# Kernel optimization log

Hardware: AMD Instinct MI355X
Metric: run time of the kernel (lower is better)

The kernel has to match this reference:

```python
import jax, jax.numpy as jnp
import numpy as np

NUM_JOINTS = 24
NUM_THETAS = NUM_JOINTS * 3  # 72
NUM_VERTS = 6890
NUM_BETAS = 10
BATCH = 512

SMPL_PARENTS = np.array([0, 0, 0, 0, 1, 2, 3, 4, 5, 6, 7, 8, 9, 9, 9,
                         12, 13, 14, 16, 17, 18, 19, 20, 21], dtype=np.int32)


def setup_inputs() -> dict:
    key = jax.random.key(0)
    ks = jax.random.split(key, 6)
    x = jax.random.normal(ks[0], (BATCH, NUM_THETAS + NUM_BETAS), dtype=jnp.float32) * 0.3
    v_template = jax.random.normal(ks[1], (NUM_VERTS, 3), dtype=jnp.float32) * 0.3
    shapedirs = jax.random.normal(ks[2], (NUM_BETAS, NUM_VERTS * 3), dtype=jnp.float32) * 0.01
    posedirs = jax.random.normal(ks[3], (207, NUM_VERTS * 3), dtype=jnp.float32) * 0.001
    Jr = jax.random.uniform(ks[4], (NUM_VERTS, NUM_JOINTS), dtype=jnp.float32)
    J_regressor = Jr / jnp.sum(Jr, axis=0, keepdims=True)
    W = jax.random.uniform(ks[5], (NUM_VERTS, NUM_JOINTS), dtype=jnp.float32)
    lbs_weights = W / jnp.sum(W, axis=1, keepdims=True)  # rows sum to 1 (skinning weights)
    parents = jnp.asarray(SMPL_PARENTS)
    return {"x": x, "v_template": v_template, "shapedirs": shapedirs,
            "J_regressor": J_regressor, "posedirs": posedirs,
            "lbs_weights": lbs_weights, "parents": parents}


def batch_rodrigues(theta):
    # theta: [N,3] axis-angle -> [N,3,3] rotation matrices
    angle = jnp.linalg.norm(theta + 1e-8, axis=1, keepdims=True)  # [N,1]
    r = theta / angle                                              # [N,3] unit axis
    cos = jnp.cos(angle)[..., None]                                # [N,1,1]
    sin = jnp.sin(angle)[..., None]
    outer = r[:, :, None] * r[:, None, :]                          # [N,3,3]
    rx, ry, rz = r[:, 0], r[:, 1], r[:, 2]
    zero = jnp.zeros_like(rx)
    K = jnp.stack([zero, -rz, ry,
                   rz, zero, -rx,
                   -ry, rx, zero], axis=1).reshape(-1, 3, 3)       # skew-symmetric
    eye = jnp.eye(3, dtype=theta.dtype)
    return cos * eye + (1.0 - cos) * outer + sin * K


def global_rigid_transformation(Rs, J, parents):
    # Rs: [B,24,3,3], J: [B,24,3] -> A: [B,24,4,4]
    B = Rs.shape[0]
    dtype = Rs.dtype
    bottom = jnp.broadcast_to(jnp.array([0, 0, 0, 1], dtype=dtype), (B, 1, 4))

    def make_A(R, t):  # R:[B,3,3], t:[B,3]
        Rt = jnp.concatenate([R, t[:, :, None]], axis=2)  # [B,3,4]
        return jnp.concatenate([Rt, bottom], axis=1)       # [B,4,4]

    parents = np.asarray(parents)
    results = [make_A(Rs[:, 0], J[:, 0])]
    for i in range(1, NUM_JOINTS):
        t_rel = J[:, i] - J[:, parents[i]]
        A_here = make_A(Rs[:, i], t_rel)
        results.append(jnp.matmul(results[parents[i]], A_here))
    results = jnp.stack(results, axis=1)  # [B,24,4,4]

    Js_w0 = jnp.concatenate([J, jnp.zeros((B, NUM_JOINTS, 1), dtype=dtype)], axis=2)  # [B,24,4]
    init_bone = jnp.einsum('bjpq,bjq->bjp', results, Js_w0)                           # [B,24,4]
    A = results - jnp.pad(init_bone[..., None], ((0, 0), (0, 0), (0, 0), (3, 0)))
    return A


def reference(x, v_template, shapedirs, J_regressor, posedirs, lbs_weights, parents):
    B = x.shape[0]
    thetas = x[:, :NUM_THETAS]
    betas = x[:, NUM_THETAS:]

    # shape blendshapes
    v_shaped = (betas @ shapedirs).reshape(B, NUM_VERTS, 3) + v_template  # [B,V,3]

    J = jnp.einsum('bvc,vj->bjc', v_shaped, J_regressor)  # [B,24,3]

    # pose rotations + pose blendshapes
    Rs = batch_rodrigues(thetas.reshape(-1, 3)).reshape(B, NUM_JOINTS, 3, 3)
    pose_feature = (Rs[:, 1:] - jnp.eye(3, dtype=x.dtype)).reshape(B, 207)
    v_posed = (pose_feature @ posedirs).reshape(B, NUM_VERTS, 3) + v_shaped

    # kinematic chain
    A = global_rigid_transformation(Rs, J, parents)  # [B,24,4,4]

    # linear blend skinning
    T = jnp.einsum('vj,bjpq->bvpq', lbs_weights, A)  # [B,V,4,4]
    v_posed_homo = jnp.concatenate(
        [v_posed, jnp.ones((B, NUM_VERTS, 1), dtype=x.dtype)], axis=2)  # [B,V,4]
    verts = jnp.einsum('bvpq,bvq->bvp', T, v_posed_homo)[:, :, :3]
    return verts
```

## Files before the change

kernel.cpp:

```cpp
#include <hip/hip_runtime.h>

#define NUM_JOINTS 24
#define NUM_VERTS  6890
#define NUM_COORDS (NUM_VERTS * 3)
#define NUM_BETAS  10
#define KTOT       217
#define KPAD       224
#define BATCH      512
#define VPAD       6912

#define WS_SJP  0
#define WS_XBF  85536
#define WS_DBF  142880
#define WS_WHBF 2465312
#define WS_AH   2575904
#define WS_AL   2706976

typedef __attribute__((ext_vector_type(8))) short short8;
typedef __attribute__((ext_vector_type(4))) float f32x4;

__device__ inline unsigned short f2bf(float f) {
    union { float f; unsigned u; } c; c.f = f;
    unsigned u = c.u;
    u += 0x7fffu + ((u >> 16) & 1u);
    return (unsigned short)(u >> 16);
}
__device__ inline float bf2f(unsigned short h) {
    union { unsigned u; float f; } c; c.u = ((unsigned)h) << 16;
    return c.f;
}

struct PBShm {
    float Rs[4][24][9];
    float Jl[4][24][3];
    float Rg[4][24][9];
    float tg[4][24][3];
    float As[4][24][12];
};

__global__ __launch_bounds__(256) void k_prep(const float* __restrict__ Jr,
                                              const float* __restrict__ sd,
                                              const float* __restrict__ pd,
                                              const float* __restrict__ vt,
                                              const float* __restrict__ w,
                                              float* __restrict__ ws) {
    __shared__ __align__(16) unsigned char smem[28928];
    const int t   = blockIdx.x;
    const int tid = threadIdx.x;
    unsigned short* whbf = (unsigned short*)(ws + WS_WHBF);
    unsigned short* dbf  = (unsigned short*)(ws + WS_DBF);

    if (t < 27) {
        const int v = t * 256 + tid;
        const bool ok = (v < NUM_VERTS);
        unsigned short row[32];
        #pragma unroll
        for (int j = 0; j < 32; ++j)
            row[j] = f2bf((ok && j < 24) ? w[v * 24 + j] : 0.f);
        #pragma unroll
        for (int i = 0; i < 4; ++i)
            *(float4*)(whbf + (size_t)v * 32 + i * 8) = *(const float4*)(&row[i * 8]);
    } else if (t < 351) {
        unsigned* L = (unsigned*)smem;
        const int c0   = (t - 27) * 64;
        const int lane = tid & 63;
        const int grp  = tid >> 6;
        const int c    = c0 + lane;
        const bool cv  = (c < NUM_COORDS);
        #pragma unroll 4
        for (int i = 0; i < 28; ++i) {
            const int p  = i * 4 + grp;
            const int k0 = 2 * p, k1 = k0 + 1;
            float v0 = 0.f, v1 = 0.f;
            if (cv) {
                v0 = (k0 < 10) ? sd[(size_t)k0 * NUM_COORDS + c]
                   : (k0 < KTOT) ? pd[(size_t)(k0 - 10) * NUM_COORDS + c] : 0.f;
                v1 = (k1 < 10) ? sd[(size_t)k1 * NUM_COORDS + c]
                   : (k1 < KTOT) ? pd[(size_t)(k1 - 10) * NUM_COORDS + c] : 0.f;
            }
            L[lane * 113 + p] = (unsigned)f2bf(v0) | ((unsigned)f2bf(v1) << 16);
        }
        __syncthreads();
        #pragma unroll
        for (int i = 0; i < 7; ++i) {
            const int idx = i * 256 + tid;
            const int row = idx / 28;
            const int q   = idx % 28;
            uint4 val;
            val.x = L[row * 113 + q * 4 + 0];
            val.y = L[row * 113 + q * 4 + 1];
            val.z = L[row * 113 + q * 4 + 2];
            val.w = L[row * 113 + q * 4 + 3];
            *(uint4*)(dbf + (size_t)(c0 + row) * KPAD + q * 8) = val;
        }
    } else {
        float* Jl = (float*)smem;
        float* S  = (float*)smem + 64 * 25;
        const int strip = t - 351;
        const int v0 = strip * 64;
        #pragma unroll
        for (int i = 0; i < 6; ++i) {
            const int idx = i * 256 + tid;
            const int v = idx / 24, j = idx % 24;
            Jl[v * 25 + j] = (v0 + v < NUM_VERTS) ? Jr[(size_t)(v0 + v) * 24 + j] : 0.f;
        }
        #pragma unroll
        for (int i = 0; i < 9; ++i) {
            const int idx = i * 256 + tid;
            if (idx < 33 * 64) {
                const int s = idx / 64, v = idx % 64;
                float val = 0.f;
                if (v0 + v < NUM_VERTS) {
                    if (s < 30) val = sd[(size_t)(s / 3) * NUM_COORDS + (size_t)(v0 + v) * 3 + (s % 3)];
                    else        val = vt[(size_t)(v0 + v) * 3 + (s - 30)];
                }
                S[s * 64 + v] = val;
            }
        }
        __syncthreads();
        float* wsp = ws + WS_SJP + (size_t)strip * 792;
        for (int o = tid; o < 792; o += 256) {
            const int s = o / 24, j = o % 24;
            float sum = 0.f;
            #pragma unroll 8
            for (int v = 0; v < 64; ++v)
                sum += S[s * 64 + v] * Jl[v * 25 + j];
            wsp[o] = sum;
        }
    }
}

__global__ __launch_bounds__(256) void k_pb(const float* __restrict__ x,
                                            const int* __restrict__ parents,
                                            float* __restrict__ ws) {
    __shared__ PBShm P;
    __shared__ float SJf[792];
    unsigned short* xbf = (unsigned short*)(ws + WS_XBF);
    unsigned short* ahi = (unsigned short*)(ws + WS_AH);
    unsigned short* alo = (unsigned short*)(ws + WS_AL);
    const int tid = threadIdx.x;

    {
        const float* wsp = ws + WS_SJP;
        for (int o = tid; o < 792; o += 256) {
            float sum = 0.f;
            for (int s2 = 0; s2 < 108; ++s2)
                sum += wsp[(size_t)s2 * 792 + o];
            SJf[o] = sum;
        }
    }
    __syncthreads();

    const int sub  = tid >> 6;
    const int lane = tid & 63;
    const int b = blockIdx.x * 4 + sub;
    const float* row = x + b * (NUM_BETAS + 72);

    if (lane < 24) {
        const int j = lane;
        const float t0 = row[3 * j + 0], t1 = row[3 * j + 1], t2 = row[3 * j + 2];
        const float a0 = t0 + 1e-8f, a1 = t1 + 1e-8f, a2 = t2 + 1e-8f;
        const float angle = sqrtf(a0 * a0 + a1 * a1 + a2 * a2);
        const float inv = 1.0f / angle;
        const float rx = t0 * inv, ry = t1 * inv, rz = t2 * inv;
        const float c = cosf(angle), sn = sinf(angle), o = 1.f - c;
        float R[9];
        R[0] = c + o * rx * rx;       R[1] = o * rx * ry - sn * rz; R[2] = o * rx * rz + sn * ry;
        R[3] = o * rx * ry + sn * rz; R[4] = c + o * ry * ry;       R[5] = o * ry * rz - sn * rx;
        R[6] = o * rx * rz - sn * ry; R[7] = o * ry * rz + sn * rx; R[8] = c + o * rz * rz;
        #pragma unroll
        for (int i = 0; i < 9; ++i) P.Rs[sub][j][i] = R[i];
        #pragma unroll
        for (int c3 = 0; c3 < 3; ++c3) {
            float s = SJf[(30 + c3) * 24 + j];
            #pragma unroll
            for (int k = 0; k < NUM_BETAS; ++k)
                s += row[72 + k] * SJf[(k * 3 + c3) * 24 + j];
            P.Jl[sub][j][c3] = s;
        }
        if (j >= 1) {
            #pragma unroll
            for (int i = 0; i < 9; ++i) {
                const float pf = R[i] - ((i == 0 || i == 4 || i == 8) ? 1.f : 0.f);
                xbf[(size_t)b * KPAD + 10 + (j - 1) * 9 + i] = f2bf(pf);
            }
        }
    }
    if (lane < NUM_BETAS) xbf[(size_t)b * KPAD + lane] = f2bf(row[72 + lane]);
    if (lane == 63) {
        #pragma unroll
        for (int k = KTOT; k < KPAD; ++k) xbf[(size_t)b * KPAD + k] = 0;
    }
    __syncthreads();

    if (lane == 0) {
        #pragma unroll
        for (int i = 0; i < 9; ++i) P.Rg[sub][0][i] = P.Rs[sub][0][i];
        #pragma unroll
        for (int c3 = 0; c3 < 3; ++c3) P.tg[sub][0][c3] = P.Jl[sub][0][c3];
        for (int i = 1; i < 24; ++i) {
            const int p = parents[i];
            float tmp[9];
            #pragma unroll
            for (int r = 0; r < 3; ++r)
                #pragma unroll
                for (int cc = 0; cc < 3; ++cc)
                    tmp[r * 3 + cc] = P.Rg[sub][p][r * 3 + 0] * P.Rs[sub][i][0 + cc] +
                                      P.Rg[sub][p][r * 3 + 1] * P.Rs[sub][i][3 + cc] +
                                      P.Rg[sub][p][r * 3 + 2] * P.Rs[sub][i][6 + cc];
            #pragma unroll
            for (int q = 0; q < 9; ++q) P.Rg[sub][i][q] = tmp[q];
            const float tr0 = P.Jl[sub][i][0] - P.Jl[sub][p][0];
            const float tr1 = P.Jl[sub][i][1] - P.Jl[sub][p][1];
            const float tr2 = P.Jl[sub][i][2] - P.Jl[sub][p][2];
            #pragma unroll
            for (int r = 0; r < 3; ++r)
                P.tg[sub][i][r] = P.Rg[sub][p][r * 3 + 0] * tr0 + P.Rg[sub][p][r * 3 + 1] * tr1 +
                                  P.Rg[sub][p][r * 3 + 2] * tr2 + P.tg[sub][p][r];
        }
    }
    __syncthreads();

    if (lane < 24) {
        const int j = lane;
        #pragma unroll
        for (int r = 0; r < 3; ++r) {
            const float tt = P.tg[sub][j][r] - (P.Rg[sub][j][r * 3 + 0] * P.Jl[sub][j][0] +
                                                P.Rg[sub][j][r * 3 + 1] * P.Jl[sub][j][1] +
                                                P.Rg[sub][j][r * 3 + 2] * P.Jl[sub][j][2]);
            P.As[sub][j][r * 4 + 0] = P.Rg[sub][j][r * 3 + 0];
            P.As[sub][j][r * 4 + 1] = P.Rg[sub][j][r * 3 + 1];
            P.As[sub][j][r * 4 + 2] = P.Rg[sub][j][r * 3 + 2];
            P.As[sub][j][r * 4 + 3] = tt;
        }
    }
    __syncthreads();

    if (lane < 32) {
        const int r = lane >> 1;
        const int half = lane & 1;
        unsigned short hi[16], lo[16];
        #pragma unroll
        for (int i = 0; i < 16; ++i) {
            const int j = half * 16 + i;
            float v = 0.f;
            if (r < 12 && j < 24) v = P.As[sub][j][r];
            const unsigned short h = f2bf(v);
            hi[i] = h;
            lo[i] = f2bf(v - bf2f(h));
        }
        unsigned short* dh = ahi + ((size_t)b * 16 + r) * 32 + half * 16;
        unsigned short* dl = alo + ((size_t)b * 16 + r) * 32 + half * 16;
        #pragma unroll
        for (int i = 0; i < 2; ++i) {
            *(float4*)(dh + i * 8) = *(const float4*)(&hi[i * 8]);
            *(float4*)(dl + i * 8) = *(const float4*)(&lo[i * 8]);
        }
    }
}

__global__ __launch_bounds__(256) void k_gemmA(const float* __restrict__ vt,
                                               float* __restrict__ out,
                                               float* __restrict__ ws) {
    __shared__ __align__(16) unsigned short Xs[32 * 232];
    const unsigned short* dbf = (const unsigned short*)(ws + WS_DBF);
    const unsigned short* xbf = (const unsigned short*)(ws + WS_XBF);
    const int tid  = threadIdx.x;
    const int wave = tid >> 6;
    const int lane = tid & 63;
    const int col  = lane & 15;
    const int quad = lane >> 4;
    const int c0   = blockIdx.x * 192;

    short8 bfrag[3][7];
    float vtl[3];
    #pragma unroll
    for (int nt = 0; nt < 3; ++nt) {
        const int nc = c0 + wave * 48 + nt * 16 + col;
        const unsigned short* brow = dbf + (size_t)nc * KPAD + quad * 8;
        #pragma unroll
        for (int kb = 0; kb < 7; ++kb)
            bfrag[nt][kb] = *(const short8*)(brow + kb * 32);
        vtl[nt] = (nc < NUM_COORDS) ? vt[nc] : 0.f;
    }

    for (int chunk = 0; chunk < 4; ++chunk) {
        const int m0 = blockIdx.y * 128 + chunk * 32;
        __syncthreads();
        #pragma unroll
        for (int i = 0; i < 4; ++i) {
            const int c = tid + i * 256;
            if (c < 32 * 28) {
                const int r = c / 28, off = c % 28;
                *(float4*)(&Xs[r * 232 + off * 8]) =
                    *(const float4*)(xbf + (size_t)(m0 + r) * KPAD + off * 8);
            }
        }
        __syncthreads();

        #pragma unroll
        for (int mt = 0; mt < 2; ++mt) {
            const unsigned short* arow = &Xs[(mt * 16 + col) * 232 + quad * 8];
            f32x4 acc[3] = {{0.f,0.f,0.f,0.f},{0.f,0.f,0.f,0.f},{0.f,0.f,0.f,0.f}};
            #pragma unroll
            for (int kb = 0; kb < 7; ++kb) {
                const short8 af = *(const short8*)(arow + kb * 32);
                #pragma unroll
                for (int nt = 0; nt < 3; ++nt)
                    acc[nt] = __builtin_amdgcn_mfma_f32_16x16x32_bf16(af, bfrag[nt][kb], acc[nt], 0, 0, 0);
            }
            #pragma unroll
            for (int nt = 0; nt < 3; ++nt) {
                const int nc = c0 + wave * 48 + nt * 16 + col;
                if (nc < NUM_COORDS) {
                    float* base = out + (size_t)(m0 + mt * 16 + quad * 4) * NUM_COORDS + nc;
                    base[0]                      = acc[nt][0] + vtl[nt];
                    base[(size_t)NUM_COORDS]     = acc[nt][1] + vtl[nt];
                    base[(size_t)2 * NUM_COORDS] = acc[nt][2] + vtl[nt];
                    base[(size_t)3 * NUM_COORDS] = acc[nt][3] + vtl[nt];
                }
            }
        }
    }
}

__global__ __launch_bounds__(256) void k_skin(float* __restrict__ out,
                                              float* __restrict__ ws) {
    __shared__ __align__(16) float Ts[4][64 * 20];
    const unsigned short* whbf = (const unsigned short*)(ws + WS_WHBF);
    const unsigned short* ahi  = (const unsigned short*)(ws + WS_AH);
    const unsigned short* alo  = (const unsigned short*)(ws + WS_AL);
    const int tid  = threadIdx.x;
    const int wave = tid >> 6;
    const int lane = tid & 63;
    const int col  = lane & 15;
    const int quad = lane >> 4;
    const int v0   = blockIdx.x * 64;
    const int b0   = blockIdx.y * 64;

    short8 wfrag[4];
    #pragma unroll
    for (int mt = 0; mt < 4; ++mt)
        wfrag[mt] = *(const short8*)(whbf + (size_t)(v0 + mt * 16 + col) * 32 + quad * 8);

    float* ts = &Ts[wave][0];
    const int vv = v0 + lane;
    const bool vok = (vv < NUM_VERTS);

    for (int nt = wave; nt < 64; nt += 4) {
        const int b = b0 + nt;
        float* orow = out + (size_t)b * NUM_COORDS + (size_t)vv * 3;
        float h0 = 0.f, h1 = 0.f, h2 = 0.f;
        if (vok) { h0 = orow[0]; h1 = orow[1]; h2 = orow[2]; }

        const short8 bh = *(const short8*)(ahi + ((size_t)b * 16 + col) * 32 + quad * 8);
        const short8 bl = *(const short8*)(alo + ((size_t)b * 16 + col) * 32 + quad * 8);

        f32x4 acc[4];
        #pragma unroll
        for (int mt = 0; mt < 4; ++mt) {
            f32x4 z = {0.f, 0.f, 0.f, 0.f};
            z = __builtin_amdgcn_mfma_f32_16x16x32_bf16(wfrag[mt], bh, z, 0, 0, 0);
            z = __builtin_amdgcn_mfma_f32_16x16x32_bf16(wfrag[mt], bl, z, 0, 0, 0);
            acc[mt] = z;
        }
        #pragma unroll
        for (int mt = 0; mt < 4; ++mt)
            #pragma unroll
            for (int r = 0; r < 4; ++r)
                ts[(mt * 16 + quad * 4 + r) * 20 + col] = acc[mt][r];

        const f32x4 t0 = *(const f32x4*)(ts + lane * 20 + 0);
        const f32x4 t1 = *(const f32x4*)(ts + lane * 20 + 4);
        const f32x4 t2 = *(const f32x4*)(ts + lane * 20 + 8);

        if (vok) {
            __builtin_nontemporal_store(t0[0] * h0 + t0[1] * h1 + t0[2] * h2 + t0[3], orow + 0);
            __builtin_nontemporal_store(t1[0] * h0 + t1[1] * h1 + t1[2] * h2 + t1[3], orow + 1);
            __builtin_nontemporal_store(t2[0] * h0 + t2[1] * h1 + t2[2] * h2 + t2[3], orow + 2);
        }
    }
}

extern "C" void kernel_launch(void* const* d_in, const int* in_sizes, int n_in,
                              void* d_out, int out_size, void* d_ws, size_t ws_size,
                              hipStream_t stream) {
    const float* x  = (const float*)d_in[0];
    const float* vt = (const float*)d_in[1];
    const float* sd = (const float*)d_in[2];
    const float* Jr = (const float*)d_in[3];
    const float* pd = (const float*)d_in[4];
    const float* w  = (const float*)d_in[5];
    const int* parents = (const int*)d_in[6];
    float* out = (float*)d_out;
    float* ws  = (float*)d_ws;

    k_prep <<<459, 256, 0, stream>>>(Jr, sd, pd, vt, w, ws);
    k_pb   <<<128, 256, 0, stream>>>(x, parents, ws);
    k_gemmA<<<dim3(108, 4), 256, 0, stream>>>(vt, out, ws);
    k_skin <<<dim3(108, 8), 256, 0, stream>>>(out, ws);
}
```

Measured before the change: 161.7 us.

## Fuse blendshape GEMM and skinning into one kernel with LDS-staged v_posed

Merges the pose/shape blendshape GEMM and the linear blend skinning kernels into a single kernel. Each block computes v_posed for 64 batches × 192 coords into shared memory, then skins those same 64 vertices directly from LDS. This removes the full write and re-read of the intermediate v_posed through global memory, and one kernel launch. In exchange it uses roughly 70KB of LDS per block, which may lower occupancy, and the B-fragment loads are now done by twice as many blocks.

New measurement: 158.2 us. -2.1%, faster.

```diff
diff --git a/kernel.cpp b/kernel.cpp
--- a/kernel.cpp
+++ b/kernel.cpp
@@ -259,18 +259,27 @@
     }
 }
 
-__global__ __launch_bounds__(256) void k_gemmA(const float* __restrict__ vt,
+__global__ __launch_bounds__(256) void k_fused(const float* __restrict__ vt,
                                                float* __restrict__ out,
                                                float* __restrict__ ws) {
-    __shared__ __align__(16) unsigned short Xs[32 * 232];
-    const unsigned short* dbf = (const unsigned short*)(ws + WS_DBF);
-    const unsigned short* xbf = (const unsigned short*)(ws + WS_XBF);
+    __shared__ __align__(16) float VP[64 * 194];
+    __shared__ __align__(16) unsigned char U[20480];
+    unsigned short* Xs = (unsigned short*)U;
+    float*          Tsf = (float*)U;
+
+    const unsigned short* dbf  = (const unsigned short*)(ws + WS_DBF);
+    const unsigned short* xbf  = (const unsigned short*)(ws + WS_XBF);
+    const unsigned short* whbf = (const unsigned short*)(ws + WS_WHBF);
+    const unsigned short* ahi  = (const unsigned short*)(ws + WS_AH);
+    const unsigned short* alo  = (const unsigned short*)(ws + WS_AL);
+
     const int tid  = threadIdx.x;
     const int wave = tid >> 6;
     const int lane = tid & 63;
     const int col  = lane & 15;
     const int quad = lane >> 4;
     const int c0   = blockIdx.x * 192;
+    const int b0   = blockIdx.y * 64;
 
     short8 bfrag[3][7];
     float vtl[3];
@@ -284,8 +293,8 @@
         vtl[nt] = (nc < NUM_COORDS) ? vt[nc] : 0.f;
     }
 
-    for (int chunk = 0; chunk < 4; ++chunk) {
-        const int m0 = blockIdx.y * 128 + chunk * 32;
+    for (int chunk = 0; chunk < 2; ++chunk) {
+        const int m0 = b0 + chunk * 32;
         __syncthreads();
         #pragma unroll
         for (int i = 0; i < 4; ++i) {
@@ -311,70 +320,54 @@
             }
             #pragma unroll
             for (int nt = 0; nt < 3; ++nt) {
-                const int nc = c0 + wave * 48 + nt * 16 + col;
-                if (nc < NUM_COORDS) {
-                    float* base = out + (size_t)(m0 + mt * 16 + quad * 4) * NUM_COORDS + nc;
-                    base[0]                      = acc[nt][0] + vtl[nt];
-                    base[(size_t)NUM_COORDS]     = acc[nt][1] + vtl[nt];
-                    base[(size_t)2 * NUM_COORDS] = acc[nt][2] + vtl[nt];
-                    base[(size_t)3 * NUM_COORDS] = acc[nt][3] + vtl[nt];
-                }
-            }
-        }
-    }
-}
-
-__global__ __launch_bounds__(256) void k_skin(float* __restrict__ out,
-                                              float* __restrict__ ws) {
-    __shared__ __align__(16) float Ts[4][64 * 20];
-    const unsigned short* whbf = (const unsigned short*)(ws + WS_WHBF);
-    const unsigned short* ahi  = (const unsigned short*)(ws + WS_AH);
-    const unsigned short* alo  = (const unsigned short*)(ws + WS_AL);
-    const int tid  = threadIdx.x;
-    const int wave = tid >> 6;
-    const int lane = tid & 63;
-    const int col  = lane & 15;
-    const int quad = lane >> 4;
-    const int v0   = blockIdx.x * 64;
-    const int b0   = blockIdx.y * 64;
-
+                const int cc = wave * 48 + nt * 16 + col;
+                #pragma unroll
+                for (int r = 0; r < 4; ++r)
+                    VP[(chunk * 32 + mt * 16 + quad * 4 + r) * 194 + cc] = acc[nt][r] + vtl[nt];
+            }
+        }
+    }
+    __syncthreads();
+
+    const int v0 = blockIdx.x * 64;
     short8 wfrag[4];
     #pragma unroll
     for (int mt = 0; mt < 4; ++mt)
         wfrag[mt] = *(const short8*)(whbf + (size_t)(v0 + mt * 16 + col) * 32 + quad * 8);
 
-    float* ts = &Ts[wave][0];
+    float* ts = Tsf + wave * (64 * 20);
     const int vv = v0 + lane;
     const bool vok = (vv < NUM_VERTS);
 
     for (int nt = wave; nt < 64; nt += 4) {
         const int b = b0 + nt;
-        float* orow = out + (size_t)b * NUM_COORDS + (size_t)vv * 3;
-        float h0 = 0.f, h1 = 0.f, h2 = 0.f;
-        if (vok) { h0 = orow[0]; h1 = orow[1]; h2 = orow[2]; }
-
         const short8 bh = *(const short8*)(ahi + ((size_t)b * 16 + col) * 32 + quad * 8);
         const short8 bl = *(const short8*)(alo + ((size_t)b * 16 + col) * 32 + quad * 8);
 
-        f32x4 acc[4];
+        f32x4 acc2[4];
         #pragma unroll
         for (int mt = 0; mt < 4; ++mt) {
             f32x4 z = {0.f, 0.f, 0.f, 0.f};
             z = __builtin_amdgcn_mfma_f32_16x16x32_bf16(wfrag[mt], bh, z, 0, 0, 0);
             z = __builtin_amdgcn_mfma_f32_16x16x32_bf16(wfrag[mt], bl, z, 0, 0, 0);
-            acc[mt] = z;
+            acc2[mt] = z;
         }
         #pragma unroll
         for (int mt = 0; mt < 4; ++mt)
             #pragma unroll
             for (int r = 0; r < 4; ++r)
-                ts[(mt * 16 + quad * 4 + r) * 20 + col] = acc[mt][r];
+                ts[(mt * 16 + quad * 4 + r) * 20 + col] = acc2[mt][r];
 
         const f32x4 t0 = *(const f32x4*)(ts + lane * 20 + 0);
         const f32x4 t1 = *(const f32x4*)(ts + lane * 20 + 4);
         const f32x4 t2 = *(const f32x4*)(ts + lane * 20 + 8);
 
+        const float h0 = VP[nt * 194 + lane * 3 + 0];
+        const float h1 = VP[nt * 194 + lane * 3 + 1];
+        const float h2 = VP[nt * 194 + lane * 3 + 2];
+
         if (vok) {
+            float* orow = out + (size_t)b * NUM_COORDS + (size_t)vv * 3;
             __builtin_nontemporal_store(t0[0] * h0 + t0[1] * h1 + t0[2] * h2 + t0[3], orow + 0);
             __builtin_nontemporal_store(t1[0] * h0 + t1[1] * h1 + t1[2] * h2 + t1[3], orow + 1);
             __builtin_nontemporal_store(t2[0] * h0 + t2[1] * h1 + t2[2] * h2 + t2[3], orow + 2);
@@ -397,6 +390,5 @@
 
     k_prep <<<459, 256, 0, stream>>>(Jr, sd, pd, vt, w, ws);
     k_pb   <<<128, 256, 0, stream>>>(x, parents, ws);
-    k_gemmA<<<dim3(108, 4), 256, 0, stream>>>(vt, out, ws);
-    k_skin <<<dim3(108, 8), 256, 0, stream>>>(out, ws);
-}
+    k_fused<<<dim3(108, 8), 256, 0, stream>>>(vt, out, ws);
+}
```
